# Optimization experiments

Hardware: AMD Instinct MI355X
Metric: run time of the kernel (lower is better)

## Reference

```python
import jax, jax.numpy as jnp
import numpy as np
import math

B, C_IN, H, W_DIM, D_DIM = 2, 128, 24, 24, 24
D_MODEL, N_HEAD, N_LAYERS, D_FF = 256, 8, 4, 512
D_K = D_MODEL // N_HEAD
EPS = 1e-6


def setup_inputs() -> dict:
    key = jax.random.key(0)
    ks = jax.random.split(key, 16)
    s = 0.02
    inp = {
        "x": jax.random.normal(ks[0], (B, C_IN, H, W_DIM, D_DIM), jnp.float32),
        # 1x1x1 Conv3d W_x: weight [out, in], bias [out]
        "Wx_w": jax.random.normal(ks[1], (D_MODEL, C_IN), jnp.float32) * s,
        "Wx_b": jnp.zeros((D_MODEL,), jnp.float32),
        # per-layer attention projections (stacked over layers)
        "Wq": jax.random.normal(ks[2], (N_LAYERS, D_MODEL, D_MODEL), jnp.float32) * s,
        "bq": jnp.zeros((N_LAYERS, D_MODEL), jnp.float32),
        "Wk": jax.random.normal(ks[3], (N_LAYERS, D_MODEL, D_MODEL), jnp.float32) * s,
        "bk": jnp.zeros((N_LAYERS, D_MODEL), jnp.float32),
        "Wv": jax.random.normal(ks[4], (N_LAYERS, D_MODEL, D_MODEL), jnp.float32) * s,
        "bv": jnp.zeros((N_LAYERS, D_MODEL), jnp.float32),
        "Wo": jax.random.normal(ks[5], (N_LAYERS, D_MODEL, D_MODEL), jnp.float32) * s,
        "bo": jnp.zeros((N_LAYERS, D_MODEL), jnp.float32),
        # layer norms
        "ln1_g": jnp.ones((N_LAYERS, D_MODEL), jnp.float32),
        "ln1_b": jnp.zeros((N_LAYERS, D_MODEL), jnp.float32),
        "ln2_g": jnp.ones((N_LAYERS, D_MODEL), jnp.float32),
        "ln2_b": jnp.zeros((N_LAYERS, D_MODEL), jnp.float32),
        # FFN
        "ffn_w1": jax.random.normal(ks[6], (N_LAYERS, D_MODEL, D_FF), jnp.float32) * s,
        "ffn_b1": jnp.zeros((N_LAYERS, D_FF), jnp.float32),
        "ffn_w2": jax.random.normal(ks[7], (N_LAYERS, D_FF, D_MODEL), jnp.float32) * s,
        "ffn_b2": jnp.zeros((N_LAYERS, D_MODEL), jnp.float32),
        # depthwise 3x3x3 conv positional encoder (groups = D_MODEL)
        "pos_w": jax.random.normal(ks[8], (N_LAYERS, D_MODEL, 1, 3, 3, 3), jnp.float32) * s,
        "pos_b": jnp.zeros((N_LAYERS, D_MODEL), jnp.float32),
    }
    return inp


def _layer_norm(t, g, b):
    mu = jnp.mean(t, axis=-1, keepdims=True)
    var = jnp.var(t, axis=-1, keepdims=True)
    return (t - mu) * jax.lax.rsqrt(var + EPS) * g + b


def reference(x, Wx_w, Wx_b, Wq, bq, Wk, bk, Wv, bv, Wo, bo,
              ln1_g, ln1_b, ln2_g, ln2_b,
              ffn_w1, ffn_b1, ffn_w2, ffn_b2, pos_w, pos_b):
    b = x.shape[0]
    # 1x1x1 conv projection W_x + ReLU (is_up=False path)
    x = jnp.einsum('bchwd,oc->bohwd', x, Wx_w) + Wx_b[None, :, None, None, None]
    x = jax.nn.relu(x)

    inv_sqrt_dk = 1.0 / math.sqrt(D_K)

    for i in range(N_LAYERS):
        # flatten spatial -> tokens: [b, n, d_model]
        t = jnp.transpose(x.reshape(b, D_MODEL, -1), (0, 2, 1))
        n = t.shape[1]

        def heads(y):  # [b,n,d] -> [b,h,n,dk]
            return jnp.transpose(y.reshape(b, n, N_HEAD, D_K), (0, 2, 1, 3))

        q = heads(t @ Wq[i] + bq[i])
        k = heads(t @ Wk[i] + bk[i])
        v = heads(t @ Wv[i] + bv[i])

        # linear attention: softmax over feature dim for q, token dim for k
        q = jax.nn.softmax(q, axis=-1) * inv_sqrt_dk
        k = jax.nn.softmax(k, axis=-2)
        ctx = jnp.einsum('bhnd,bhne->bhde', k, v)     # [b,h,dk,dk]
        o = jnp.einsum('bhnd,bhde->bhne', q, ctx)      # [b,h,n,dk]
        o = jnp.transpose(o, (0, 2, 1, 3)).reshape(b, n, D_MODEL)
        o = o @ Wo[i] + bo[i]

        t = _layer_norm(t + o, ln1_g[i], ln1_b[i])
        f = jax.nn.gelu(t @ ffn_w1[i] + ffn_b1[i], approximate=False) @ ffn_w2[i] + ffn_b2[i]
        t = _layer_norm(t + f, ln2_g[i], ln2_b[i])

        # back to volume and depthwise conv positional embedding
        x = jnp.transpose(t, (0, 2, 1)).reshape(b, D_MODEL, H, W_DIM, D_DIM)
        pos = jax.lax.conv_general_dilated(
            x, pos_w[i], window_strides=(1, 1, 1), padding='SAME',
            dimension_numbers=('NCDHW', 'OIDHW', 'NCDHW'),
            feature_group_count=D_MODEL,
        ) + pos_b[i][None, :, None, None, None]
        x = x + pos
    return x
```

## Files before the change

### kernel.cpp

```cpp
#include <hip/hip_runtime.h>
#include <math.h>

#define NTOK 13824
#define MTOT 27648
#define BATCH 2
#define CIN 128
#define DMODEL 256
#define NHEAD 8
#define NLAYERS 4
#define DFF 512
#define NSPLIT 27
#define KVHALF ((size_t)BATCH * 256 * NTOK)

typedef float f32x4 __attribute__((ext_vector_type(4)));
typedef __bf16 bf16x8 __attribute__((ext_vector_type(8)));
typedef __attribute__((address_space(1))) void gvoid;
typedef __attribute__((address_space(3))) void lvoid;

#define GLDS16(g, l) __builtin_amdgcn_global_load_lds((gvoid*)(g), (lvoid*)(l), 16, 0, 0)

__device__ __forceinline__ unsigned short f2bf(float f) {
    unsigned u = __float_as_uint(f);
    return (unsigned short)((u + 0x7FFFu + ((u >> 16) & 1u)) >> 16);
}
__device__ __forceinline__ float bf2f(unsigned short h) {
    return __uint_as_float(((unsigned)h) << 16);
}

template<int ACT, int OUTM>
__global__ __launch_bounds__(256) void gemm_bf16(
    const unsigned short* __restrict__ A, int lda,
    const unsigned short* __restrict__ Bt, int ldb,
    const float* __restrict__ bias,
    float* __restrict__ Cf, unsigned short* __restrict__ Cb,
    int ldc, int K, long sA, long sB, long sC)
{
    A  += (size_t)blockIdx.z * sA;
    Bt += (size_t)blockIdx.z * sB;
    if (OUTM == 2) Cf += (size_t)blockIdx.z * sC;
    Cb += (size_t)blockIdx.z * sC;

    __shared__ __attribute__((aligned(16))) unsigned short As[2][8192];
    __shared__ __attribute__((aligned(16))) unsigned short Bs[2][8192];
    const int t    = threadIdx.x;
    const int lane = t & 63;
    const int wave = t >> 6;
    const int wm = wave & 1, wn = wave >> 1;
    const int m0 = blockIdx.x * 128, n0 = blockIdx.y * 128;

    const int srow = t >> 3;
    const int skid = ((t & 7) * 8) ^ ((srow & 7) << 3);
    const unsigned short* ga = A  + (size_t)(m0 + srow) * lda + skid;
    const unsigned short* gb = Bt + (size_t)(n0 + srow) * ldb + skid;

    f32x4 acc[4][4];
    #pragma unroll
    for (int i = 0; i < 4; ++i)
        #pragma unroll
        for (int j = 0; j < 4; ++j) acc[i][j] = (f32x4)0.0f;

    const int fm  = lane & 15;
    const int fq8 = (lane >> 4) * 8;
    const int sw3 = (fm & 7) << 3;
    const int arow = (wm * 64 + fm) * 64;
    const int brow = (wn * 64 + fm) * 64;

#define STAGE(bufi, kk)                                                        \
    {                                                                          \
        _Pragma("unroll")                                                      \
        for (int p = 0; p < 4; ++p) {                                          \
            GLDS16(ga + (size_t)p * 32 * lda + (kk), &As[bufi][p * 2048 + t * 8]); \
            GLDS16(gb + (size_t)p * 32 * ldb + (kk), &Bs[bufi][p * 2048 + t * 8]); \
        }                                                                      \
    }

#define COMPUTE(bufi)                                                          \
    {                                                                          \
        _Pragma("unroll")                                                      \
        for (int ks = 0; ks < 2; ++ks) {                                       \
            bf16x8 af[4], bg[4];                                               \
            const int kidx = (fq8 + ks * 32) ^ sw3;                            \
            _Pragma("unroll")                                                  \
            for (int i = 0; i < 4; ++i)                                        \
                af[i] = *(const bf16x8*)(&As[bufi][arow + i * 1024 + kidx]);   \
            _Pragma("unroll")                                                  \
            for (int j = 0; j < 4; ++j)                                        \
                bg[j] = *(const bf16x8*)(&Bs[bufi][brow + j * 1024 + kidx]);   \
            _Pragma("unroll")                                                  \
            for (int i = 0; i < 4; ++i)                                        \
                _Pragma("unroll")                                              \
                for (int j = 0; j < 4; ++j)                                    \
                    acc[i][j] = __builtin_amdgcn_mfma_f32_16x16x32_bf16(       \
                        af[i], bg[j], acc[i][j], 0, 0, 0);                     \
        }                                                                      \
    }

    STAGE(0, 0)
    __syncthreads();
    const int NT = K >> 6;
    int cur = 0;
    for (int t64 = 0; t64 < NT - 1; ++t64) {
        STAGE(cur ^ 1, (t64 + 1) * 64)
        COMPUTE(cur)
        __syncthreads();
        cur ^= 1;
    }
    COMPUTE(cur)

#undef STAGE
#undef COMPUTE

    const int cb  = n0 + wn * 64 + fm;
    const int rbs = m0 + wm * 64 + (lane >> 4) * 4;
    #pragma unroll
    for (int j = 0; j < 4; ++j) {
        const int n = cb + j * 16;
        const float bv = bias[n];
        #pragma unroll
        for (int i = 0; i < 4; ++i) {
            #pragma unroll
            for (int r = 0; r < 4; ++r) {
                float v = acc[i][j][r] + bv;
                if (ACT == 1) v = fmaxf(v, 0.0f);
                if (ACT == 2) v = 0.5f * v * (1.0f + erff(v * 0.7071067811865476f));
                const size_t off = (size_t)(rbs + i * 16 + r) * ldc + n;
                if (OUTM == 2) Cf[off] = v;
                Cb[off] = f2bf(v);
            }
        }
    }
}

#define CW_QKV  786432
#define CW_O   1048576
#define CW_1   1572864
#define CW_2   2097152
#define CW_X   2129920
#define CW_B   2132992
__global__ __launch_bounds__(256) void conv_weights(
    const float* __restrict__ Wq, const float* __restrict__ Wk,
    const float* __restrict__ Wv, const float* __restrict__ Wo,
    const float* __restrict__ fw1, const float* __restrict__ fw2,
    const float* __restrict__ Wx_w,
    const float* __restrict__ bq, const float* __restrict__ bk,
    const float* __restrict__ bv,
    unsigned short* __restrict__ wqkv_t, unsigned short* __restrict__ wo_t,
    unsigned short* __restrict__ w1_t, unsigned short* __restrict__ w2_t,
    unsigned short* __restrict__ wx_bf, float* __restrict__ bqkv)
{
    const int e = blockIdx.x * 256 + threadIdx.x;
    if (e < CW_QKV) {
        const int i = e / 196608, r = e % 196608;
        const int n = r / 256, k = r % 256;
        const float* src = (n < 256) ? Wq : (n < 512) ? Wk : Wv;
        wqkv_t[e] = f2bf(src[((size_t)i * 256 + k) * 256 + (n & 255)]);
    } else if (e < CW_O) {
        const int r = e - CW_QKV;
        const int i = r / 65536, rr = r % 65536, n = rr / 256, k = rr % 256;
        wo_t[r] = f2bf(Wo[((size_t)i * 256 + k) * 256 + n]);
    } else if (e < CW_1) {
        const int r = e - CW_O;
        const int i = r / 131072, rr = r % 131072, n = rr / 256, k = rr % 256;
        w1_t[r] = f2bf(fw1[((size_t)i * 256 + k) * 512 + n]);
    } else if (e < CW_2) {
        const int r = e - CW_1;
        const int i = r / 131072, rr = r % 131072, n = rr / 512, k = rr % 512;
        w2_t[r] = f2bf(fw2[((size_t)i * 512 + k) * 256 + n]);
    } else if (e < CW_X) {
        const int r = e - CW_2;
        wx_bf[r] = f2bf(Wx_w[r]);
    } else if (e < CW_B) {
        const int r = e - CW_X;
        const int i = r / 768, j = r % 768;
        const float v = (j < 256) ? bq[i * 256 + j]
                      : (j < 512) ? bk[i * 256 + j - 256]
                                  : bv[i * 256 + j - 512];
        bqkv[r] = v;
    }
}

__global__ __launch_bounds__(256) void conv_x(
    const float* __restrict__ x, unsigned short* __restrict__ xbf)
{
    __shared__ float tile[32][33];
    const int n0 = blockIdx.x * 32;
    const int c0 = blockIdx.y * 32;
    const int b  = blockIdx.z;
    const int t = threadIdx.x;
    const int tn = t & 31, tc = t >> 5;
    #pragma unroll
    for (int p = 0; p < 4; ++p)
        tile[tc + p * 8][tn] =
            x[((size_t)(b * CIN + c0 + tc + p * 8)) * NTOK + n0 + tn];
    __syncthreads();
    const int cc = t & 31, nr = t >> 5;
    #pragma unroll
    for (int p = 0; p < 4; ++p)
        xbf[((size_t)(b * NTOK + n0 + nr + p * 8)) * CIN + c0 + cc] =
            f2bf(tile[cc][nr + p * 8]);
}

__global__ __launch_bounds__(256) void qsm_kernel(unsigned short* __restrict__ qkv)
{
    const int g = blockIdx.x * 256 + threadIdx.x;
    const int row = g >> 5;
    const int cg  = g & 31;
    unsigned short* p = qkv + (size_t)row * 768 + cg * 8;
    uint4 raw = *(const uint4*)p;
    unsigned short* rp = (unsigned short*)&raw;
    float v[8];
    #pragma unroll
    for (int j = 0; j < 8; ++j) v[j] = bf2f(rp[j]);
    float m = v[0];
    #pragma unroll
    for (int j = 1; j < 8; ++j) m = fmaxf(m, v[j]);
    m = fmaxf(m, __shfl_xor(m, 1, 64));
    m = fmaxf(m, __shfl_xor(m, 2, 64));
    float s = 0.0f;
    #pragma unroll
    for (int j = 0; j < 8; ++j) { v[j] = __expf(v[j] - m); s += v[j]; }
    s += __shfl_xor(s, 1, 64);
    s += __shfl_xor(s, 2, 64);
    const float r = 1.0f / s;
    #pragma unroll
    for (int j = 0; j < 8; ++j) rp[j] = f2bf(v[j] * r);
    *(uint4*)p = raw;
}

__global__ __launch_bounds__(256) void kvt_kernel(
    const unsigned short* __restrict__ qkv, unsigned short* __restrict__ kvT)
{
    const int nb = blockIdx.x, h = blockIdx.y, b = blockIdx.z;
    const int n0 = nb * 64;
    const int t = threadIdx.x;
    __shared__ __attribute__((aligned(16))) unsigned short LT[64 * 72];
    const int tl = t >> 2, cg = t & 3;
    const unsigned short* src =
        qkv + ((size_t)(b * NTOK + n0 + tl)) * 768 + 256 + h * 32 + cg * 8;
    const uint4 kr = *(const uint4*)src;
    const uint4 vr = *(const uint4*)(src + 256);
    const unsigned short* ks = (const unsigned short*)&kr;
    const unsigned short* vs = (const unsigned short*)&vr;
    #pragma unroll
    for (int j = 0; j < 8; ++j) {
        const int ch = cg * 8 + j;
        LT[ch * 72 + tl]        = f2bf(__expf(bf2f(ks[j])));
        LT[(32 + ch) * 72 + tl] = vs[j];
    }
    __syncthreads();
    #pragma unroll
    for (int it = 0; it < 2; ++it) {
        const int idx = it * 256 + t;
        const int row = idx >> 3, seg = idx & 7;
        const uint4 val = *(const uint4*)(LT + row * 72 + seg * 8);
        const int ch = row & 31;
        const size_t dst = ((row >= 32) ? KVHALF : (size_t)0)
                         + ((size_t)(b * 256 + h * 32 + ch)) * NTOK + n0 + seg * 8;
        *(uint4*)(kvT + dst) = val;
    }
}

__global__ __launch_bounds__(256) void ctx_mfma(
    const unsigned short* __restrict__ kvT,
    float* __restrict__ ctxp, float* __restrict__ skp)
{
    const int s = blockIdx.x, h = blockIdx.y, b = blockIdx.z;
    const int t = threadIdx.x, w = t >> 6, l = t & 63;
    const int fm = l & 15, fq = (l >> 4) * 8;
    const size_t rowA = (size_t)(b * 256 + h * 32 + fm) * NTOK;
    const int n0 = s * 512 + w * 128 + fq;
    const unsigned short* pa = kvT + rowA + n0;
    const unsigned short* pb = kvT + KVHALF + rowA + n0;

    f32x4 acc[2][2];
    #pragma unroll
    for (int x = 0; x < 2; ++x)
        #pragma unroll
        for (int y = 0; y < 2; ++y) acc[x][y] = (f32x4)0.0f;
    float ss0 = 0.0f, ss1 = 0.0f;

    #pragma unroll
    for (int step = 0; step < 4; ++step) {
        const int ko = step * 32;
        const uint4 ra0 = *(const uint4*)(pa + ko);
        const uint4 ra1 = *(const uint4*)(pa + (size_t)16 * NTOK + ko);
        const uint4 rb0 = *(const uint4*)(pb + ko);
        const uint4 rb1 = *(const uint4*)(pb + (size_t)16 * NTOK + ko);
        const bf16x8 a0 = *(const bf16x8*)&ra0;
        const bf16x8 a1 = *(const bf16x8*)&ra1;
        const bf16x8 b0 = *(const bf16x8*)&rb0;
        const bf16x8 b1 = *(const bf16x8*)&rb1;
        acc[0][0] = __builtin_amdgcn_mfma_f32_16x16x32_bf16(a0, b0, acc[0][0], 0, 0, 0);
        acc[0][1] = __builtin_amdgcn_mfma_f32_16x16x32_bf16(a0, b1, acc[0][1], 0, 0, 0);
        acc[1][0] = __builtin_amdgcn_mfma_f32_16x16x32_bf16(a1, b0, acc[1][0], 0, 0, 0);
        acc[1][1] = __builtin_amdgcn_mfma_f32_16x16x32_bf16(a1, b1, acc[1][1], 0, 0, 0);
        const unsigned short* u0 = (const unsigned short*)&ra0;
        const unsigned short* u1 = (const unsigned short*)&ra1;
        #pragma unroll
        for (int j = 0; j < 8; ++j) { ss0 += bf2f(u0[j]); ss1 += bf2f(u1[j]); }
    }

    ss0 += __shfl_xor(ss0, 16, 64); ss0 += __shfl_xor(ss0, 32, 64);
    ss1 += __shfl_xor(ss1, 16, 64); ss1 += __shfl_xor(ss1, 32, 64);
    __shared__ float skw[4][32];
    __shared__ float redc[4][32][33];
    if (l < 16) { skw[w][fm] = ss0; skw[w][16 + fm] = ss1; }

    const int rb4 = (l >> 4) * 4;
    #pragma unroll
    for (int x = 0; x < 2; ++x)
        #pragma unroll
        for (int y = 0; y < 2; ++y)
            #pragma unroll
            for (int r = 0; r < 4; ++r)
                redc[w][x * 16 + rb4 + r][y * 16 + fm] = acc[x][y][r];
    __syncthreads();

    if (t < 32)
        skp[(size_t)s * 512 + b * 256 + h * 32 + t] =
            skw[0][t] + skw[1][t] + skw[2][t] + skw[3][t];

    const int e0 = t * 4;
    const int dd = e0 >> 5, c0 = e0 & 31;
    float4 o;
    o.x = redc[0][dd][c0+0] + redc[1][dd][c0+0] + redc[2][dd][c0+0] + redc[3][dd][c0+0];
    o.y = redc[0][dd][c0+1] + redc[1][dd][c0+1] + redc[2][dd][c0+1] + redc[3][dd][c0+1];
    o.z = redc[0][dd][c0+2] + redc[1][dd][c0+2] + redc[2][dd][c0+2] + redc[3][dd][c0+2];
    o.w = redc[0][dd][c0+3] + redc[1][dd][c0+3] + redc[2][dd][c0+3] + redc[3][dd][c0+3];
    *(float4*)(ctxp + ((size_t)s * 16 + b * 8 + h) * 1024 + e0) = o;
}

__global__ __launch_bounds__(256) void ctxred(
    const float* __restrict__ ctxp, const float* __restrict__ skp,
    float* __restrict__ ctx, float* __restrict__ Sk)
{
    const int o = blockIdx.x * 256 + threadIdx.x;
    if (o < 16384) {
        float a = 0.0f;
        for (int s = 0; s < NSPLIT; ++s) a += ctxp[(size_t)s * 16384 + o];
        ctx[o] = a;
    } else {
        const int c = o - 16384;
        float a = 0.0f;
        for (int s = 0; s < NSPLIT; ++s) a += skp[(size_t)s * 512 + c];
        Sk[c] = a;
    }
}

__global__ __launch_bounds__(256) void ctxwo_kernel(
    const float* __restrict__ ctx, const float* __restrict__ Sk,
    const unsigned short* __restrict__ wo_t, unsigned short* __restrict__ wp)
{
    const int h = blockIdx.x, b = blockIdx.y;
    const int n = threadIdx.x;
    __shared__ float cl[1024];
    __shared__ float sdk[32];
    {
        const float* cp = ctx + (size_t)(b * 8 + h) * 1024;
        *(float4*)&cl[n * 4] = *(const float4*)&cp[n * 4];
    }
    if (n < 32) sdk[n] = 0.17677669529663687f / Sk[b * 256 + h * 32 + n];
    __syncthreads();
    float w[32];
    const unsigned short* wop = wo_t + (size_t)n * 256 + h * 32;
    #pragma unroll
    for (int e = 0; e < 32; ++e) w[e] = bf2f(wop[e]);
    unsigned short outv[32];
    #pragma unroll
    for (int d = 0; d < 32; ++d) {
        float acc = 0.0f;
        #pragma unroll
        for (int e = 0; e < 32; ++e) acc += cl[d * 32 + e] * w[e];
        outv[d] = f2bf(acc * sdk[d]);
    }
    unsigned short* op = wp + (size_t)b * 65536 + (size_t)n * 256 + h * 32;
    #pragma unroll
    for (int d = 0; d < 32; d += 8)
        *(uint4*)(op + d) = *(uint4*)(outv + d);
}

template<int WB>
__global__ __launch_bounds__(256) void ln_kernel(
    float* __restrict__ t, const unsigned short* __restrict__ add,
    const float* __restrict__ g, const float* __restrict__ bta,
    unsigned short* __restrict__ tbf)
{
    const int row = blockIdx.x;
    const int c = threadIdx.x;
    const int lane = c & 63, wave = c >> 6;
    const size_t off = (size_t)row * 256 + c;
    const float v = t[off] + bf2f(add[off]);
    __shared__ float red[8];
    float s = v;
    #pragma unroll
    for (int o = 32; o; o >>= 1) s += __shfl_xor(s, o, 64);
    if (lane == 0) red[wave] = s;
    __syncthreads();
    const float mu = (red[0] + red[1] + red[2] + red[3]) * (1.0f / 256.0f);
    const float dv = v - mu;
    float s2 = dv * dv;
    #pragma unroll
    for (int o = 32; o; o >>= 1) s2 += __shfl_xor(s2, o, 64);
    if (lane == 0) red[wave + 4] = s2;
    __syncthreads();
    const float var = (red[4] + red[5] + red[6] + red[7]) * (1.0f / 256.0f);
    const float o = dv * rsqrtf(var + 1e-6f) * g[c] + bta[c];
    t[off] = o;
    if (WB) tbf[off] = f2bf(o);
}

template<int WB>
__global__ __launch_bounds__(256) void posconv_kernel(
    const float* __restrict__ tin, const float* __restrict__ pw,
    const float* __restrict__ pb, float* __restrict__ outp,
    unsigned short* __restrict__ tbfp)
{
    const int hw = blockIdx.x;
    const int b  = blockIdx.y;
    const int hh = hw / 24, ww = hw % 24;
    const int c  = threadIdx.x;

    float w[27];
    #pragma unroll
    for (int k = 0; k < 27; ++k) w[k] = pw[c * 27 + k];
    const float bias = pb[c];

    const float* base = tin + (size_t)b * NTOK * 256 + c;

    const float* colp[9];
    bool colok[9];
    #pragma unroll
    for (int dh = -1; dh <= 1; ++dh)
        #pragma unroll
        for (int dw = -1; dw <= 1; ++dw) {
            const int j = (dh + 1) * 3 + (dw + 1);
            const int h2 = hh + dh, w2 = ww + dw;
            colok[j] = ((unsigned)h2 < 24u) & ((unsigned)w2 < 24u);
            colp[j] = base + (size_t)((h2 * 24 + w2) * 24) * 256;
        }

    float win[9][3];
    #pragma unroll
    for (int j = 0; j < 9; ++j) {
        win[j][0] = 0.0f;
        win[j][1] = colok[j] ? colp[j][0] : 0.0f;
    }

    float* ob = outp + ((size_t)b * NTOK + (size_t)hw * 24) * 256 + c;
    unsigned short* tb = WB ? (tbfp + ((size_t)b * NTOK + (size_t)hw * 24) * 256 + c)
                            : (unsigned short*)nullptr;

    for (int d = 0; d < 24; ++d) {
        #pragma unroll
        for (int j = 0; j < 9; ++j)
            win[j][2] = (colok[j] && d < 23) ? colp[j][(d + 1) * 256] : 0.0f;

        float acc = bias + win[4][1];
        #pragma unroll
        for (int j = 0; j < 9; ++j) {
            acc += w[j * 3 + 0] * win[j][0];
            acc += w[j * 3 + 1] * win[j][1];
            acc += w[j * 3 + 2] * win[j][2];
        }
        ob[d * 256] = acc;
        if (WB) tb[d * 256] = f2bf(acc);

        #pragma unroll
        for (int j = 0; j < 9; ++j) { win[j][0] = win[j][1]; win[j][1] = win[j][2]; }
    }
}

__global__ __launch_bounds__(256) void tr_out(
    const float* __restrict__ tin, float* __restrict__ outp)
{
    __shared__ float tile[32][33];
    const int m0 = blockIdx.x * 32;
    const int c0 = blockIdx.y * 32;
    const int t = threadIdx.x;
    const int tc = t & 31, tr = t >> 5;
    #pragma unroll
    for (int r = 0; r < 4; ++r)
        tile[tr + r * 8][tc] = tin[(size_t)(m0 + tr + r * 8) * 256 + c0 + tc];
    __syncthreads();
    const int b = (m0 >= NTOK) ? 1 : 0;
    const int n0 = m0 - b * NTOK;
    #pragma unroll
    for (int r = 0; r < 4; ++r)
        outp[((size_t)b * 256 + c0 + tr + r * 8) * NTOK + n0 + tc] = tile[tc][tr + r * 8];
}

extern "C" void kernel_launch(void* const* d_in, const int* in_sizes, int n_in,
                              void* d_out, int out_size, void* d_ws, size_t ws_size,
                              hipStream_t stream)
{
    (void)in_sizes; (void)n_in; (void)out_size; (void)ws_size;
    const float* x     = (const float*)d_in[0];
    const float* Wx_w  = (const float*)d_in[1];
    const float* Wx_b  = (const float*)d_in[2];
    const float* Wq    = (const float*)d_in[3];
    const float* bq    = (const float*)d_in[4];
    const float* Wk    = (const float*)d_in[5];
    const float* bk    = (const float*)d_in[6];
    const float* Wv    = (const float*)d_in[7];
    const float* bv    = (const float*)d_in[8];
    const float* Wo    = (const float*)d_in[9];
    const float* bo    = (const float*)d_in[10];
    const float* ln1_g = (const float*)d_in[11];
    const float* ln1_b = (const float*)d_in[12];
    const float* ln2_g = (const float*)d_in[13];
    const float* ln2_b = (const float*)d_in[14];
    const float* fw1   = (const float*)d_in[15];
    const float* fb1   = (const float*)d_in[16];
    const float* fw2   = (const float*)d_in[17];
    const float* fb2   = (const float*)d_in[18];
    const float* pw    = (const float*)d_in[19];
    const float* pb    = (const float*)d_in[20];
    float* out = (float*)d_out;

    char* p = (char*)d_ws;
    float* tA            = (float*)p;          p += (size_t)MTOT * 256 * 4;
    float* tB            = (float*)p;          p += (size_t)MTOT * 256 * 4;
    unsigned short* tbf  = (unsigned short*)p; p += (size_t)MTOT * 256 * 2;
    unsigned short* qkv  = (unsigned short*)p; p += (size_t)MTOT * 768 * 2;
    unsigned short* hbf  = (unsigned short*)p; p += (size_t)MTOT * 512 * 2;
    unsigned short* ob   = (unsigned short*)p; p += (size_t)MTOT * 256 * 2;
    unsigned short* xbf  = (unsigned short*)p; p += (size_t)MTOT * 128 * 2;
    unsigned short* wqkv_t = (unsigned short*)p; p += (size_t)786432 * 2;
    unsigned short* wo_t   = (unsigned short*)p; p += (size_t)262144 * 2;
    unsigned short* w1_t   = (unsigned short*)p; p += (size_t)524288 * 2;
    unsigned short* w2_t   = (unsigned short*)p; p += (size_t)524288 * 2;
    unsigned short* wx_bf  = (unsigned short*)p; p += (size_t)32768 * 2;
    unsigned short* wp     = (unsigned short*)p; p += (size_t)BATCH * 65536 * 2;
    float* bqkv = (float*)p; p += 3072 * 4;
    float* ctx  = (float*)p; p += 16384 * 4;
    float* Sk   = (float*)p; p += 512 * 4;
    float* ctxp = (float*)p; p += (size_t)NSPLIT * 16384 * 4;
    float* skp  = (float*)p; p += (size_t)NSPLIT * 512 * 4;
    unsigned short* kvT = hbf;

    hipLaunchKernelGGL(conv_weights, dim3(8333), dim3(256), 0, stream,
                       Wq, Wk, Wv, Wo, fw1, fw2, Wx_w, bq, bk, bv,
                       wqkv_t, wo_t, w1_t, w2_t, wx_bf, bqkv);
    hipLaunchKernelGGL(conv_x, dim3(NTOK / 32, CIN / 32, BATCH), dim3(256), 0, stream,
                       x, xbf);

    hipLaunchKernelGGL((gemm_bf16<1, 2>), dim3(216, 2, 1), dim3(256), 0, stream,
                       xbf, CIN, wx_bf, CIN, Wx_b, tA, tbf, 256, CIN,
                       (long)0, (long)0, (long)0);

    for (int i = 0; i < NLAYERS; ++i) {
        float* tin  = (i & 1) ? tB : tA;
        float* tout = (i & 1) ? tA : tB;

        hipLaunchKernelGGL((gemm_bf16<0, 1>), dim3(216, 6, 1), dim3(256), 0, stream,
                           tbf, 256, wqkv_t + (size_t)i * 196608, 256,
                           bqkv + i * 768, nullptr, qkv, 768, 256,
                           (long)0, (long)0, (long)0);

        hipLaunchKernelGGL(kvt_kernel, dim3(NTOK / 64, NHEAD, BATCH), dim3(256), 0, stream,
                           qkv, kvT);
        hipLaunchKernelGGL(ctx_mfma, dim3(NSPLIT, NHEAD, BATCH), dim3(256), 0, stream,
                           kvT, ctxp, skp);
        hipLaunchKernelGGL(ctxred, dim3(66), dim3(256), 0, stream, ctxp, skp, ctx, Sk);

        hipLaunchKernelGGL(qsm_kernel, dim3(3456), dim3(256), 0, stream, qkv);
        hipLaunchKernelGGL(ctxwo_kernel, dim3(NHEAD, BATCH), dim3(256), 0, stream,
                           ctx, Sk, wo_t + (size_t)i * 65536, wp);

        hipLaunchKernelGGL((gemm_bf16<0, 1>), dim3(108, 2, BATCH), dim3(256), 0, stream,
                           qkv, 768, wp, 256, bo + i * 256, nullptr, ob, 256, 256,
                           (long)NTOK * 768, (long)65536, (long)NTOK * 256);

        hipLaunchKernelGGL((ln_kernel<1>), dim3(MTOT), dim3(256), 0, stream,
                           tin, ob, ln1_g + i * 256, ln1_b + i * 256, tbf);

        hipLaunchKernelGGL((gemm_bf16<2, 1>), dim3(216, 4, 1), dim3(256), 0, stream,
                           tbf, 256, w1_t + (size_t)i * 131072, 256,
                           fb1 + i * 512, nullptr, hbf, 512, 256,
                           (long)0, (long)0, (long)0);
        hipLaunchKernelGGL((gemm_bf16<0, 1>), dim3(216, 2, 1), dim3(256), 0, stream,
                           hbf, 512, w2_t + (size_t)i * 131072, 512,
                           fb2 + i * 256, nullptr, ob, 256, 512,
                           (long)0, (long)0, (long)0);
        hipLaunchKernelGGL((ln_kernel<0>), dim3(MTOT), dim3(256), 0, stream,
                           tin, ob, ln2_g + i * 256, ln2_b + i * 256, nullptr);

        if (i < NLAYERS - 1)
            hipLaunchKernelGGL((posconv_kernel<1>), dim3(576, BATCH), dim3(256), 0, stream,
                               tin, pw + (size_t)i * 6912, pb + i * 256, tout, tbf);
        else
            hipLaunchKernelGGL((posconv_kernel<0>), dim3(576, BATCH), dim3(256), 0, stream,
                               tin, pw + (size_t)i * 6912, pb + i * 256, tout, nullptr);
    }

    hipLaunchKernelGGL(tr_out, dim3(MTOT / 32, 8), dim3(256), 0, stream, tA, out);
}
```

Measured before the change: 866.8 us.

## Fuse K/V transpose into GEMM, vectorize layernorm, fuse output transpose into posconv

The K/V projection now runs as a separate transposed GEMM whose epilogue applies exp to K and writes channel-major kvT directly, which removes kvt_kernel and the 768-wide qkv buffer. Q is projected into its own 256-wide buffer. Layernorm processes 8 rows per block with vectorized loads and sub-wave shuffles instead of block-wide syncs. The last posconv writes the NCDHW output directly, which removes tr_out. GEMM block IDs are also remapped across the grid, likely to improve L2 locality. Together these cut launches and memory traffic. The new remap assumes the grid size divides evenly by 8.

```diff
diff --git a/kernel.cpp b/kernel.cpp
--- a/kernel.cpp
+++ b/kernel.cpp
@@ -40,13 +40,23 @@
     if (OUTM == 2) Cf += (size_t)blockIdx.z * sC;
     Cb += (size_t)blockIdx.z * sC;
 
+    int bx, by;
+    {
+        const int nx  = gridDim.x;
+        const int q   = (nx * gridDim.y) >> 3;
+        const int lin = blockIdx.y * nx + blockIdx.x;
+        const int wg  = (lin & 7) * q + (lin >> 3);
+        bx = wg % nx;
+        by = wg / nx;
+    }
+
     __shared__ __attribute__((aligned(16))) unsigned short As[2][8192];
     __shared__ __attribute__((aligned(16))) unsigned short Bs[2][8192];
     const int t    = threadIdx.x;
     const int lane = t & 63;
     const int wave = t >> 6;
     const int wm = wave & 1, wn = wave >> 1;
-    const int m0 = blockIdx.x * 128, n0 = blockIdx.y * 128;
+    const int m0 = bx * 128, n0 = by * 128;
 
     const int srow = t >> 3;
     const int skid = ((t & 7) * 8) ^ ((srow & 7) << 3);
@@ -109,6 +119,29 @@
 
 #undef STAGE
 #undef COMPUTE
+
+    if constexpr (ACT == 3) {
+        const int cb  = n0 + wn * 64 + fm;
+        const int rbs = m0 + wm * 64 + (lane >> 4) * 4;
+        #pragma unroll
+        for (int i = 0; i < 4; ++i) {
+            #pragma unroll
+            for (int r = 0; r < 4; ++r) {
+                const int row = rbs + i * 16 + r;
+                const float bv = bias[row];
+                const size_t base = (row < 256)
+                    ? (size_t)row * NTOK
+                    : KVHALF + (size_t)(row - 256) * NTOK;
+                #pragma unroll
+                for (int j = 0; j < 4; ++j) {
+                    float v = acc[i][j][r] + bv;
+                    if (row < 256) v = __expf(v);
+                    Cb[base + cb + j * 16] = f2bf(v);
+                }
+            }
+        }
+        return;
+    }
 
     const int cb  = n0 + wn * 64 + fm;
     const int rbs = m0 + wm * 64 + (lane >> 4) * 4;
@@ -200,12 +233,12 @@
             f2bf(tile[cc][nr + p * 8]);
 }
 
-__global__ __launch_bounds__(256) void qsm_kernel(unsigned short* __restrict__ qkv)
+__global__ __launch_bounds__(256) void qsm_kernel(unsigned short* __restrict__ qbuf)
 {
     const int g = blockIdx.x * 256 + threadIdx.x;
     const int row = g >> 5;
     const int cg  = g & 31;
-    unsigned short* p = qkv + (size_t)row * 768 + cg * 8;
+    unsigned short* p = qbuf + (size_t)row * 256 + cg * 8;
     uint4 raw = *(const uint4*)p;
     unsigned short* rp = (unsigned short*)&raw;
     float v[8];
@@ -225,39 +258,6 @@
     #pragma unroll
     for (int j = 0; j < 8; ++j) rp[j] = f2bf(v[j] * r);
     *(uint4*)p = raw;
-}
-
-__global__ __launch_bounds__(256) void kvt_kernel(
-    const unsigned short* __restrict__ qkv, unsigned short* __restrict__ kvT)
-{
-    const int nb = blockIdx.x, h = blockIdx.y, b = blockIdx.z;
-    const int n0 = nb * 64;
-    const int t = threadIdx.x;
-    __shared__ __attribute__((aligned(16))) unsigned short LT[64 * 72];
-    const int tl = t >> 2, cg = t & 3;
-    const unsigned short* src =
-        qkv + ((size_t)(b * NTOK + n0 + tl)) * 768 + 256 + h * 32 + cg * 8;
-    const uint4 kr = *(const uint4*)src;
-    const uint4 vr = *(const uint4*)(src + 256);
-    const unsigned short* ks = (const unsigned short*)&kr;
-    const unsigned short* vs = (const unsigned short*)&vr;
-    #pragma unroll
-    for (int j = 0; j < 8; ++j) {
-        const int ch = cg * 8 + j;
-        LT[ch * 72 + tl]        = f2bf(__expf(bf2f(ks[j])));
-        LT[(32 + ch) * 72 + tl] = vs[j];
-    }
-    __syncthreads();
-    #pragma unroll
-    for (int it = 0; it < 2; ++it) {
-        const int idx = it * 256 + t;
-        const int row = idx >> 3, seg = idx & 7;
-        const uint4 val = *(const uint4*)(LT + row * 72 + seg * 8);
-        const int ch = row & 31;
-        const size_t dst = ((row >= 32) ? KVHALF : (size_t)0)
-                         + ((size_t)(b * 256 + h * 32 + ch)) * NTOK + n0 + seg * 8;
-        *(uint4*)(kvT + dst) = val;
-    }
 }
 
 __global__ __launch_bounds__(256) void ctx_mfma(
@@ -380,33 +380,56 @@
 }
 
 template<int WB>
-__global__ __launch_bounds__(256) void ln_kernel(
+__global__ __launch_bounds__(256) void ln8_kernel(
     float* __restrict__ t, const unsigned short* __restrict__ add,
     const float* __restrict__ g, const float* __restrict__ bta,
     unsigned short* __restrict__ tbf)
 {
-    const int row = blockIdx.x;
-    const int c = threadIdx.x;
-    const int lane = c & 63, wave = c >> 6;
-    const size_t off = (size_t)row * 256 + c;
-    const float v = t[off] + bf2f(add[off]);
-    __shared__ float red[8];
-    float s = v;
-    #pragma unroll
-    for (int o = 32; o; o >>= 1) s += __shfl_xor(s, o, 64);
-    if (lane == 0) red[wave] = s;
-    __syncthreads();
-    const float mu = (red[0] + red[1] + red[2] + red[3]) * (1.0f / 256.0f);
-    const float dv = v - mu;
-    float s2 = dv * dv;
-    #pragma unroll
-    for (int o = 32; o; o >>= 1) s2 += __shfl_xor(s2, o, 64);
-    if (lane == 0) red[wave + 4] = s2;
-    __syncthreads();
-    const float var = (red[4] + red[5] + red[6] + red[7]) * (1.0f / 256.0f);
-    const float o = dv * rsqrtf(var + 1e-6f) * g[c] + bta[c];
-    t[off] = o;
-    if (WB) tbf[off] = f2bf(o);
+    const int l  = threadIdx.x & 31;
+    const int rg = threadIdx.x >> 5;
+    const size_t row = (size_t)blockIdx.x * 8 + rg;
+    const size_t off = row * 256 + l * 8;
+
+    const float4 a0 = *(const float4*)(t + off);
+    const float4 a1 = *(const float4*)(t + off + 4);
+    const uint4  ad = *(const uint4*)(add + off);
+    const unsigned short* ap = (const unsigned short*)&ad;
+
+    float v[8] = {a0.x, a0.y, a0.z, a0.w, a1.x, a1.y, a1.z, a1.w};
+    float s = 0.0f;
+    #pragma unroll
+    for (int k = 0; k < 8; ++k) { v[k] += bf2f(ap[k]); s += v[k]; }
+    #pragma unroll
+    for (int o = 16; o; o >>= 1) s += __shfl_xor(s, o, 32);
+    const float mu = s * (1.0f / 256.0f);
+
+    float s2 = 0.0f;
+    #pragma unroll
+    for (int k = 0; k < 8; ++k) { v[k] -= mu; s2 += v[k] * v[k]; }
+    #pragma unroll
+    for (int o = 16; o; o >>= 1) s2 += __shfl_xor(s2, o, 32);
+    const float rs = rsqrtf(s2 * (1.0f / 256.0f) + 1e-6f);
+
+    const float4 g0 = *(const float4*)(g + l * 8);
+    const float4 g1 = *(const float4*)(g + l * 8 + 4);
+    const float4 b0 = *(const float4*)(bta + l * 8);
+    const float4 b1 = *(const float4*)(bta + l * 8 + 4);
+    const float gg[8] = {g0.x, g0.y, g0.z, g0.w, g1.x, g1.y, g1.z, g1.w};
+    const float bb[8] = {b0.x, b0.y, b0.z, b0.w, b1.x, b1.y, b1.z, b1.w};
+
+    float o8[8];
+    #pragma unroll
+    for (int k = 0; k < 8; ++k) o8[k] = v[k] * rs * gg[k] + bb[k];
+
+    *(float4*)(t + off)     = make_float4(o8[0], o8[1], o8[2], o8[3]);
+    *(float4*)(t + off + 4) = make_float4(o8[4], o8[5], o8[6], o8[7]);
+    if (WB) {
+        uint4 ob_;
+        unsigned short* op = (unsigned short*)&ob_;
+        #pragma unroll
+        for (int k = 0; k < 8; ++k) op[k] = f2bf(o8[k]);
+        *(uint4*)(tbf + off) = ob_;
+    }
 }
 
 template<int WB>
@@ -446,9 +469,36 @@
         win[j][1] = colok[j] ? colp[j][0] : 0.0f;
     }
 
+    if constexpr (WB == 2) {
+        float o24[24];
+        #pragma unroll
+        for (int d = 0; d < 24; ++d) {
+            #pragma unroll
+            for (int j = 0; j < 9; ++j)
+                win[j][2] = (colok[j] && d < 23) ? colp[j][(d + 1) * 256] : 0.0f;
+            float acc = bias + win[4][1];
+            #pragma unroll
+            for (int j = 0; j < 9; ++j) {
+                acc += w[j * 3 + 0] * win[j][0];
+                acc += w[j * 3 + 1] * win[j][1];
+                acc += w[j * 3 + 2] * win[j][2];
+            }
+            o24[d] = acc;
+            #pragma unroll
+            for (int j = 0; j < 9; ++j) { win[j][0] = win[j][1]; win[j][1] = win[j][2]; }
+        }
+        float* op = outp + ((size_t)b * 256 + c) * NTOK + hw * 24;
+        #pragma unroll
+        for (int q = 0; q < 6; ++q)
+            *(float4*)(op + q * 4) =
+                make_float4(o24[q*4], o24[q*4+1], o24[q*4+2], o24[q*4+3]);
+        return;
+    }
+
     float* ob = outp + ((size_t)b * NTOK + (size_t)hw * 24) * 256 + c;
-    unsigned short* tb = WB ? (tbfp + ((size_t)b * NTOK + (size_t)hw * 24) * 256 + c)
-                            : (unsigned short*)nullptr;
+    unsigned short* tb = (WB == 1)
+        ? (tbfp + ((size_t)b * NTOK + (size_t)hw * 24) * 256 + c)
+        : (unsigned short*)nullptr;
 
     for (int d = 0; d < 24; ++d) {
         #pragma unroll
@@ -463,30 +513,11 @@
             acc += w[j * 3 + 2] * win[j][2];
         }
         ob[d * 256] = acc;
-        if (WB) tb[d * 256] = f2bf(acc);
+        if (WB == 1) tb[d * 256] = f2bf(acc);
 
         #pragma unroll
         for (int j = 0; j < 9; ++j) { win[j][0] = win[j][1]; win[j][1] = win[j][2]; }
     }
-}
-
-__global__ __launch_bounds__(256) void tr_out(
-    const float* __restrict__ tin, float* __restrict__ outp)
-{
-    __shared__ float tile[32][33];
-    const int m0 = blockIdx.x * 32;
-    const int c0 = blockIdx.y * 32;
-    const int t = threadIdx.x;
-    const int tc = t & 31, tr = t >> 5;
-    #pragma unroll
-    for (int r = 0; r < 4; ++r)
-        tile[tr + r * 8][tc] = tin[(size_t)(m0 + tr + r * 8) * 256 + c0 + tc];
-    __syncthreads();
-    const int b = (m0 >= NTOK) ? 1 : 0;
-    const int n0 = m0 - b * NTOK;
-    #pragma unroll
-    for (int r = 0; r < 4; ++r)
-        outp[((size_t)b * 256 + c0 + tr + r * 8) * NTOK + n0 + tc] = tile[tc][tr + r * 8];
 }
 
 extern "C" void kernel_launch(void* const* d_in, const int* in_sizes, int n_in,
@@ -521,7 +552,7 @@
     float* tA            = (float*)p;          p += (size_t)MTOT * 256 * 4;
     float* tB            = (float*)p;          p += (size_t)MTOT * 256 * 4;
     unsigned short* tbf  = (unsigned short*)p; p += (size_t)MTOT * 256 * 2;
-    unsigned short* qkv  = (unsigned short*)p; p += (size_t)MTOT * 768 * 2;
+    unsigned short* qbuf = (unsigned short*)p; p += (size_t)MTOT * 256 * 2;
     unsigned short* hbf  = (unsigned short*)p; p += (size_t)MTOT * 512 * 2;
     unsigned short* ob   = (unsigned short*)p; p += (size_t)MTOT * 256 * 2;
     unsigned short* xbf  = (unsigned short*)p; p += (size_t)MTOT * 128 * 2;
@@ -552,26 +583,30 @@
         float* tin  = (i & 1) ? tB : tA;
         float* tout = (i & 1) ? tA : tB;
 
-        hipLaunchKernelGGL((gemm_bf16<0, 1>), dim3(216, 6, 1), dim3(256), 0, stream,
+        hipLaunchKernelGGL((gemm_bf16<0, 1>), dim3(216, 2, 1), dim3(256), 0, stream,
                            tbf, 256, wqkv_t + (size_t)i * 196608, 256,
-                           bqkv + i * 768, nullptr, qkv, 768, 256,
+                           bqkv + i * 768, nullptr, qbuf, 256, 256,
                            (long)0, (long)0, (long)0);
 
-        hipLaunchKernelGGL(kvt_kernel, dim3(NTOK / 64, NHEAD, BATCH), dim3(256), 0, stream,
-                           qkv, kvT);
+        hipLaunchKernelGGL((gemm_bf16<3, 1>), dim3(4, 108, BATCH), dim3(256), 0, stream,
+                           wqkv_t + (size_t)i * 196608 + 65536, 256,
+                           tbf, 256, bqkv + i * 768 + 256,
+                           nullptr, kvT, 0, 256,
+                           (long)0, (long)NTOK * 256, (long)256 * NTOK);
+
         hipLaunchKernelGGL(ctx_mfma, dim3(NSPLIT, NHEAD, BATCH), dim3(256), 0, stream,
                            kvT, ctxp, skp);
         hipLaunchKernelGGL(ctxred, dim3(66), dim3(256), 0, stream, ctxp, skp, ctx, Sk);
 
-        hipLaunchKernelGGL(qsm_kernel, dim3(3456), dim3(256), 0, stream, qkv);
+        hipLaunchKernelGGL(qsm_kernel, dim3(3456), dim3(256), 0, stream, qbuf);
         hipLaunchKernelGGL(ctxwo_kernel, dim3(NHEAD, BATCH), dim3(256), 0, stream,
                            ctx, Sk, wo_t + (size_t)i * 65536, wp);
 
         hipLaunchKernelGGL((gemm_bf16<0, 1>), dim3(108, 2, BATCH), dim3(256), 0, stream,
-                           qkv, 768, wp, 256, bo + i * 256, nullptr, ob, 256, 256,
-                           (long)NTOK * 768, (long)65536, (long)NTOK * 256);
-
-        hipLaunchKernelGGL((ln_kernel<1>), dim3(MTOT), dim3(256), 0, stream,
+                           qbuf, 256, wp, 256, bo + i * 256, nullptr, ob, 256, 256,
+                           (long)NTOK * 256, (long)65536, (long)NTOK * 256);
+
+        hipLaunchKernelGGL((ln8_kernel<1>), dim3(MTOT / 8), dim3(256), 0, stream,
                            tin, ob, ln1_g + i * 256, ln1_b + i * 256, tbf);
 
         hipLaunchKernelGGL((gemm_bf16<2, 1>), dim3(216, 4, 1), dim3(256), 0, stream,
@@ -582,16 +617,14 @@
                            hbf, 512, w2_t + (size_t)i * 131072, 512,
                            fb2 + i * 256, nullptr, ob, 256, 512,
                            (long)0, (long)0, (long)0);
-        hipLaunchKernelGGL((ln_kernel<0>), dim3(MTOT), dim3(256), 0, stream,
+        hipLaunchKernelGGL((ln8_kernel<0>), dim3(MTOT / 8), dim3(256), 0, stream,
                            tin, ob, ln2_g + i * 256, ln2_b + i * 256, nullptr);
 
         if (i < NLAYERS - 1)
             hipLaunchKernelGGL((posconv_kernel<1>), dim3(576, BATCH), dim3(256), 0, stream,
                                tin, pw + (size_t)i * 6912, pb + i * 256, tout, tbf);
         else
-            hipLaunchKernelGGL((posconv_kernel<0>), dim3(576, BATCH), dim3(256), 0, stream,
-                               tin, pw + (size_t)i * 6912, pb + i * 256, tout, nullptr);
-    }
-
-    hipLaunchKernelGGL(tr_out, dim3(MTOT / 32, 8), dim3(256), 0, stream, tA, out);
-}
+            hipLaunchKernelGGL((posconv_kernel<2>), dim3(576, BATCH), dim3(256), 0, stream,
+                               tin, pw + (size_t)i * 6912, pb + i * 256, out, nullptr);
+    }
+}
```

Result: faster. 800.0 us (-7.7%).
